# Performance work log

Hardware: AMD Instinct MI355X
Metric: run time of the kernel (lower is better)

## Reference

```python
import jax, jax.numpy as jnp
import numpy as np

N, D, H, B = 16384, 256, 4, 64
K_EDGE, TOP_K, NUM_HOPS = 3, 5, 2
EDGE_THRESH = 0.3
EPS = 1e-8


def setup_inputs() -> dict:
    key = jax.random.key(0)
    ks = jax.random.split(key, 32)
    g = lambda i, shape, sc=1.0: jax.random.normal(ks[i], shape, jnp.float32) * sc
    # sparse-ish symmetric adjacency (avg ~33 nonzeros/row, like a pruned memory graph)
    adj = jax.random.uniform(ks[0], (N, N), jnp.float32)
    adj = adj * (jax.random.uniform(ks[1], (N, N), jnp.float32) < 0.002)
    adj = jnp.maximum(adj, adj.T)
    return dict(
        nodes=g(2, (N, D)),
        node_values=g(3, (N,)),
        adjacency=adj,
        related_pos=g(4, (B, D)),
        query=g(5, (B, D)),
        w_in=g(6, (3 * D, D), D ** -0.5),
        b_in=jnp.zeros((3 * D,), jnp.float32),
        w_out=g(7, (D, D), D ** -0.5),
        b_out=jnp.zeros((D,), jnp.float32),
        rel_w1=g(8, (2 * D, D), (2 * D) ** -0.5),
        rel_b1=jnp.zeros((D,), jnp.float32),
        rel_w2=g(9, (D, D // 2), D ** -0.5),
        rel_b2=jnp.zeros((D // 2,), jnp.float32),
        rel_w3=g(10, (D // 2, 1), (D // 2) ** -0.5),
        rel_b3=jnp.zeros((1,), jnp.float32),
        gru_w_ih=g(11, (3 * D, D), D ** -0.5),
        gru_w_hh=g(12, (3 * D, D), D ** -0.5),
        gru_b_ih=jnp.zeros((3 * D,), jnp.float32),
        gru_b_hh=jnp.zeros((3 * D,), jnp.float32),
        node_timestamps=jax.random.randint(ks[13], (N,), 0, N),
        write_idx=jax.random.randint(ks[14], (B,), 0, N),
        total_writes=N,
    )


def _l2n(x):
    return x / (jnp.linalg.norm(x, axis=-1, keepdims=True) + EPS)


def reference(nodes, node_values, adjacency, related_pos, query,
              w_in, b_in, w_out, b_out,
              rel_w1, rel_b1, rel_w2, rel_b2, rel_w3, rel_b3,
              gru_w_ih, gru_w_hh, gru_b_ih, gru_b_hh,
              node_timestamps, write_idx, total_writes):
    b, d = query.shape
    n = nodes.shape[0]
    dh = d // H
    nodes_n = _l2n(nodes)

    # ---- write path: cosine-sim top-k edge scoring + relation-encoder MLP ----
    sims_w = _l2n(related_pos) @ nodes_n.T                      # [B,N]
    _, nbr = jax.lax.top_k(sims_w, K_EDGE)                      # [B,K]
    src = nodes[write_idx]                                      # [B,D]
    dst = nodes[nbr]                                            # [B,K,D]
    comb = jnp.concatenate(
        [jnp.broadcast_to(src[:, None, :], dst.shape), dst], -1)  # [B,K,2D]
    h = jax.nn.relu(comb @ rel_w1 + rel_b1)
    h = jax.nn.relu(h @ rel_w2 + rel_b2)
    strength = jax.nn.sigmoid(h @ rel_w3 + rel_b3)[..., 0]     # [B,K]
    same = nbr == write_idx[:, None]
    old = adjacency[write_idx[:, None], nbr]
    val = jnp.where(same, old, strength)                        # skip self-edges
    adj2 = adjacency.at[write_idx[:, None], nbr].set(val)
    adj2 = adj2.at[nbr, write_idx[:, None]].set(val)            # symmetric write

    # ---- retrieval: weighted cosine similarity + top-k seeds ----
    sims = _l2n(query) @ nodes_n.T                              # [B,N]
    recency = jnp.exp(-0.01 * (total_writes - node_timestamps).astype(jnp.float32))
    weighted = sims * jax.nn.sigmoid(node_values) * recency
    _, seed = jax.lax.top_k(weighted, TOP_K)                    # [B,TOP_K]
    visited = jnp.zeros((b, n), bool).at[jnp.arange(b)[:, None], seed].set(True)

    # ---- multi-hop graph expansion over thresholded adjacency ----
    adj_bool = (adj2 > EDGE_THRESH).astype(jnp.float32)
    for _ in range(NUM_HOPS):
        visited = visited | ((visited.astype(jnp.float32) @ adj_bool) > 0)

    # ---- masked multi-head attention: query attends to visited nodes ----
    q = (query @ w_in[:d].T + b_in[:d]).reshape(b, H, dh)
    k = (nodes @ w_in[d:2 * d].T + b_in[d:2 * d]).reshape(n, H, dh)
    v = (nodes @ w_in[2 * d:].T + b_in[2 * d:]).reshape(n, H, dh)
    scores = jnp.einsum('bhd,nhd->bhn', q, k) / np.float32(np.sqrt(dh))
    scores = jnp.where(visited[:, None, :], scores, jnp.float32(-1e9))
    attn = jax.nn.softmax(scores, axis=-1)
    ctx = jnp.einsum('bhn,nhd->bhd', attn, v).reshape(b, d)
    attended = ctx @ w_out.T + b_out                            # [B,D]

    # ---- GRUCell memory evolution: x=query, h=attended ----
    gi = query @ gru_w_ih.T + gru_b_ih
    gh = attended @ gru_w_hh.T + gru_b_hh
    i_r, i_z, i_n = jnp.split(gi, 3, -1)
    h_r, h_z, h_n = jnp.split(gh, 3, -1)
    r = jax.nn.sigmoid(i_r + h_r)
    z = jax.nn.sigmoid(i_z + h_z)
    nn_ = jnp.tanh(i_n + r * h_n)
    evolved = (1.0 - z) * nn_ + z * attended                    # [B,D]
    return evolved
```

## Files before the change

kernel.cpp:

```cpp
#include <hip/hip_runtime.h>
#include <math.h>
#include <stdint.h>

#define NN 16384
#define DD 256
#define ETH 0.3f
#define EDGE_CAP (4*1024*1024)

typedef unsigned long long u64;
typedef uint32_t u32;
typedef float f32x4 __attribute__((ext_vector_type(4)));

__global__ __launch_bounds__(256) void node_stats_k(const float* __restrict__ nodes,
    const float* __restrict__ nv, const int* __restrict__ ts, const int* __restrict__ tw,
    float* __restrict__ inv_norm, float* __restrict__ sal){
  int row = blockIdx.x*4 + (threadIdx.x>>6);
  int lane = threadIdx.x & 63;
  const float4* r4 = (const float4*)(nodes + (size_t)row*DD);
  float4 v = r4[lane];
  float s = v.x*v.x+v.y*v.y+v.z*v.z+v.w*v.w;
  #pragma unroll
  for (int o=32;o>0;o>>=1) s += __shfl_down(s,o);
  if (lane==0){
    inv_norm[row] = 1.0f/(sqrtf(s)+1e-8f);
    float x = nv[row];
    float sig = 1.0f/(1.0f+expf(-x));
    float rec = expf(-0.01f*(float)(tw[0]-ts[row]));
    sal[row] = sig*rec;
  }
}

__global__ __launch_bounds__(64) void norm_qr_k(const float* __restrict__ query,
    const float* __restrict__ related, float* __restrict__ qr){
  int blk = blockIdx.x; int lane = threadIdx.x;
  const float* src = (blk<64)? (related + (size_t)blk*DD) : (query + (size_t)(blk-64)*DD);
  float4 v = ((const float4*)src)[lane];
  float s = v.x*v.x+v.y*v.y+v.z*v.z+v.w*v.w;
  #pragma unroll
  for (int o=32;o>0;o>>=1) s += __shfl_down(s,o);
  s = __shfl(s,0);
  float inv = 1.0f/(sqrtf(s)+1e-8f);
  ((float4*)(qr + (size_t)blk*DD))[lane] = make_float4(v.x*inv,v.y*inv,v.z*inv,v.w*inv);
}

#define ACC8(r) do{ \
    accA[r].x += qs*nv0.x; accA[r].y += qs*nv0.y; accA[r].z += qs*nv0.z; accA[r].w += qs*nv0.w; \
    accB[r].x += qs*nv1.x; accB[r].y += qs*nv1.y; accB[r].z += qs*nv1.z; accB[r].w += qs*nv1.w; }while(0)

template<int RM>
__global__ __launch_bounds__(256) void gemm_smallM_k(const float* __restrict__ Qm,
    const float* __restrict__ nodes, float* __restrict__ out0, float* __restrict__ out1,
    const float* __restrict__ inv_norm, const float* __restrict__ sal, int mode){
  constexpr int M = RM*32;
  constexpr int KC = 32;
  __shared__ float qk[KC*M];
  __shared__ float ndk[KC*64];
  int t = threadIdx.x;
  int qg = t>>3, ng = t&7;
  int n0 = blockIdx.x*64;
  float4 accA[RM], accB[RM];
  #pragma unroll
  for (int r=0;r<RM;r++){ accA[r]=make_float4(0,0,0,0); accB[r]=make_float4(0,0,0,0); }
  for (int kb=0; kb<DD; kb+=KC){
    if (t < M){
      const float4* src = (const float4*)(Qm + (size_t)t*DD + kb);
      #pragma unroll
      for (int i=0;i<KC/4;i++){
        float4 w = src[i];
        qk[(i*4+0)*M+t]=w.x; qk[(i*4+1)*M+t]=w.y;
        qk[(i*4+2)*M+t]=w.z; qk[(i*4+3)*M+t]=w.w;
      }
    }
    {
      int nn = t&63, kq = t>>6;
      const float4* src = (const float4*)(nodes + (size_t)(n0+nn)*DD + kb + kq*8);
      float4 a = src[0], b = src[1];
      ndk[(kq*8+0)*64+nn]=a.x; ndk[(kq*8+1)*64+nn]=a.y; ndk[(kq*8+2)*64+nn]=a.z; ndk[(kq*8+3)*64+nn]=a.w;
      ndk[(kq*8+4)*64+nn]=b.x; ndk[(kq*8+5)*64+nn]=b.y; ndk[(kq*8+6)*64+nn]=b.z; ndk[(kq*8+7)*64+nn]=b.w;
    }
    __syncthreads();
    for (int k=0;k<KC;k++){
      float4 nv0 = *(const float4*)&ndk[k*64 + ng*8];
      float4 nv1 = *(const float4*)&ndk[k*64 + ng*8 + 4];
      float4 q0  = *(const float4*)&qk[k*M + qg*RM];
      float qs;
      qs=q0.x; ACC8(0); qs=q0.y; ACC8(1); qs=q0.z; ACC8(2); qs=q0.w; ACC8(3);
      if constexpr (RM==8){
        float4 q1 = *(const float4*)&qk[k*M + qg*RM + 4];
        qs=q1.x; ACC8(4); qs=q1.y; ACC8(5); qs=q1.z; ACC8(6); qs=q1.w; ACC8(7);
      }
    }
    __syncthreads();
  }
  int nbase = n0 + ng*8;
  float4 in0, in1, sa0, sa1;
  if (mode==0){
    in0 = *(const float4*)&inv_norm[nbase]; in1 = *(const float4*)&inv_norm[nbase+4];
    sa0 = *(const float4*)&sal[nbase];      sa1 = *(const float4*)&sal[nbase+4];
  }
  #pragma unroll
  for (int r=0;r<RM;r++){
    int row = qg*RM + r;
    float4 a = accA[r], b = accB[r];
    if (mode==0){
      float4 s0 = make_float4(a.x*in0.x, a.y*in0.y, a.z*in0.z, a.w*in0.w);
      float4 s1 = make_float4(b.x*in1.x, b.y*in1.y, b.z*in1.z, b.w*in1.w);
      if (row < 64){
        *(float4*)&out0[(size_t)row*NN + nbase]     = s0;
        *(float4*)&out0[(size_t)row*NN + nbase + 4] = s1;
      } else {
        float4 w0 = make_float4(s0.x*sa0.x, s0.y*sa0.y, s0.z*sa0.z, s0.w*sa0.w);
        float4 w1 = make_float4(s1.x*sa1.x, s1.y*sa1.y, s1.z*sa1.z, s1.w*sa1.w);
        *(float4*)&out1[(size_t)(row-64)*NN + nbase]     = w0;
        *(float4*)&out1[(size_t)(row-64)*NN + nbase + 4] = w1;
      }
    } else {
      float4 s0 = make_float4(a.x*0.125f, a.y*0.125f, a.z*0.125f, a.w*0.125f);
      float4 s1 = make_float4(b.x*0.125f, b.y*0.125f, b.z*0.125f, b.w*0.125f);
      *(float4*)&out0[(size_t)row*NN + nbase]     = s0;
      *(float4*)&out0[(size_t)row*NN + nbase + 4] = s1;
    }
  }
}

__global__ __launch_bounds__(1024) void topk_k(const float* __restrict__ src, int K,
    int* __restrict__ outIdx, u64* __restrict__ vis){
  int b = blockIdx.x, t = threadIdx.x;
  const float* row = src + (size_t)b*NN;
  __shared__ float sv[1024]; __shared__ int si[1024]; __shared__ int chosen[5];
  for (int kk=0;kk<K;kk++){
    float best = -3.0e38f; int bi = NN;
    for (int n=t;n<NN;n+=1024){
      bool skip=false;
      for (int c=0;c<kk;c++) if (chosen[c]==n) skip=true;
      if (skip) continue;
      float v = row[n];
      if (v > best){ best=v; bi=n; }
    }
    sv[t]=best; si[t]=bi;
    __syncthreads();
    for (int s=512;s>0;s>>=1){
      if (t<s){
        float v2=sv[t+s]; int i2=si[t+s];
        if (v2>sv[t] || (v2==sv[t] && i2<si[t])){ sv[t]=v2; si[t]=i2; }
      }
      __syncthreads();
    }
    if (t==0){
      chosen[kk]=si[0]; outIdx[b*K+kk]=si[0];
      if (vis) atomicOr(&vis[si[0]], 1ull<<b);
    }
    __syncthreads();
  }
}

__global__ __launch_bounds__(256) void rel_patch_k(const float* __restrict__ nodes,
    const int* __restrict__ write_idx, const int* __restrict__ nbr,
    const float* __restrict__ w1, const float* __restrict__ b1,
    const float* __restrict__ w2, const float* __restrict__ b2,
    const float* __restrict__ w3, const float* __restrict__ b3,
    u32* __restrict__ modkeys, u32* __restrict__ addkeys, int* __restrict__ ctrl,
    u32* __restrict__ rowmod){
  int b = blockIdx.x, t = threadIdx.x;
  __shared__ float comb[512], h1[256], red[128];
  int w = write_idx[b];
  for (int k=0;k<3;k++){
    int nb = nbr[b*3+k];
    comb[t]     = nodes[(size_t)w*DD + t];
    comb[256+t] = nodes[(size_t)nb*DD + t];
    __syncthreads();
    float a1 = b1[t];
    for (int i=0;i<512;i++) a1 += comb[i]*w1[(size_t)i*256 + t];
    h1[t] = a1>0.f ? a1 : 0.f;
    __syncthreads();
    if (t<128){
      float a2 = b2[t];
      for (int i=0;i<256;i++) a2 += h1[i]*w2[(size_t)i*128 + t];
      float h2 = a2>0.f ? a2 : 0.f;
      red[t] = h2*w3[t];
    }
    __syncthreads();
    for (int s=64;s>0;s>>=1){ if (t<s) red[t]+=red[t+s]; __syncthreads(); }
    if (t==0 && nb != w){
      float strength = 1.0f/(1.0f+expf(-(red[0]+b3[0])));
      u32 k1 = ((u32)w<<14)|(u32)nb, k2 = ((u32)nb<<14)|(u32)w;
      int m = atomicAdd(&ctrl[1],2);
      modkeys[m]=k1; modkeys[m+1]=k2;
      if (strength > ETH){ int a=atomicAdd(&ctrl[2],2); addkeys[a]=k1; addkeys[a+1]=k2; }
      atomicOr(&rowmod[(u32)w>>5], 1u<<((u32)w&31));
      atomicOr(&rowmod[(u32)nb>>5], 1u<<((u32)nb&31));
    }
    __syncthreads();
  }
}

#define LCAP 4096
#define GITER 8
__global__ __launch_bounds__(256) void scan_adj_k(const float* __restrict__ adj,
    const u32* __restrict__ rowmod, const u32* __restrict__ modkeys,
    const int* __restrict__ ctrl, u32* __restrict__ edges, int* __restrict__ ecnt){
  __shared__ u32 lbuf[LCAP];
  __shared__ int lcnt, gbase;
  int t = threadIdx.x;
  if (t==0) lcnt = 0;
  __syncthreads();
  int nm = ctrl[1];
  size_t tid = (size_t)blockIdx.x*256 + t;
  size_t stride = (size_t)gridDim.x*256;
  const f32x4* a4 = (const f32x4*)adj;
  const size_t total4 = (size_t)NN*NN/4;
  int iters = (int)(total4 / stride);
  for (int g=0; g<iters; g+=GITER){
    f32x4 x0,x1,x2,x3,x4,x5,x6,x7;
    asm volatile("global_load_dwordx4 %0, %1, off" : "=v"(x0) : "v"(a4 + tid + (size_t)(g+0)*stride));
    asm volatile("global_load_dwordx4 %0, %1, off" : "=v"(x1) : "v"(a4 + tid + (size_t)(g+1)*stride));
    asm volatile("global_load_dwordx4 %0, %1, off" : "=v"(x2) : "v"(a4 + tid + (size_t)(g+2)*stride));
    asm volatile("global_load_dwordx4 %0, %1, off" : "=v"(x3) : "v"(a4 + tid + (size_t)(g+3)*stride));
    asm volatile("global_load_dwordx4 %0, %1, off" : "=v"(x4) : "v"(a4 + tid + (size_t)(g+4)*stride));
    asm volatile("global_load_dwordx4 %0, %1, off" : "=v"(x5) : "v"(a4 + tid + (size_t)(g+5)*stride));
    asm volatile("global_load_dwordx4 %0, %1, off" : "=v"(x6) : "v"(a4 + tid + (size_t)(g+6)*stride));
    asm volatile("global_load_dwordx4 %0, %1, off" : "=v"(x7) : "v"(a4 + tid + (size_t)(g+7)*stride));
    asm volatile("s_waitcnt vmcnt(0)" ::: "memory");
    __builtin_amdgcn_sched_barrier(0);
    #define PROC(XX, GI) do{ \
      _Pragma("unroll") \
      for (int e=0;e<4;e++){ \
        if (XX[e] > ETH){ \
          size_t li = (tid + (size_t)(g+GI)*stride)*4 + e; \
          u32 i = (u32)(li >> 14), j = (u32)(li & 16383); \
          u32 key = (i<<14)|j; \
          bool keep = true; \
          if ((rowmod[i>>5]>>(i&31))&1u){ \
            for (int c=0;c<nm;c++) if (modkeys[c]==key){ keep=false; break; } \
          } \
          if (keep){ \
            int p = atomicAdd(&lcnt, 1); \
            if (p < LCAP) lbuf[p] = key; \
            else { int d = atomicAdd(ecnt,1); if (d < EDGE_CAP) edges[d] = key; } \
          } \
        } \
      } }while(0)
    PROC(x0,0); PROC(x1,1); PROC(x2,2); PROC(x3,3);
    PROC(x4,4); PROC(x5,5); PROC(x6,6); PROC(x7,7);
    #undef PROC
  }
  __syncthreads();
  int cnt = lcnt; if (cnt > LCAP) cnt = LCAP;
  if (cnt > 0){
    if (t==0) gbase = atomicAdd(ecnt, cnt);
    __syncthreads();
    int b0 = gbase;
    for (int i=t; i<cnt; i+=256){
      int d = b0 + i;
      if (d < EDGE_CAP) edges[d] = lbuf[i];
    }
  }
}

__global__ void patch_add_k(const u32* __restrict__ addkeys, const int* __restrict__ ctrl,
    u32* __restrict__ edges, int* __restrict__ ecnt){
  if (blockIdx.x==0 && threadIdx.x==0){
    int na = ctrl[2];
    int base = atomicAdd(ecnt, na);
    for (int i=0;i<na;i++) if (base+i < EDGE_CAP) edges[base+i] = addkeys[i];
  }
}

__global__ __launch_bounds__(256) void propagate_k(const u32* __restrict__ edges,
    const int* __restrict__ ecnt, const u64* __restrict__ vin, u64* __restrict__ vout){
  int n = *ecnt; if (n > EDGE_CAP) n = EDGE_CAP;
  int tid = blockIdx.x*256 + threadIdx.x;
  int stride = gridDim.x*256;
  for (int idx=tid; idx<n; idx+=stride){
    u32 key = edges[idx];
    u32 i = key>>14, j = key & 16383u;
    u64 wv = vin[i];
    if (wv) atomicOr(&vout[j], wv);
  }
}

__global__ __launch_bounds__(256) void qproj_k(const float* __restrict__ query,
    const float* __restrict__ w_in, const float* __restrict__ b_in, float* __restrict__ qproj){
  int b = blockIdx.x, o = threadIdx.x;
  float s = b_in[o];
  const float* wr = w_in + (size_t)o*256;
  const float* q = query + (size_t)b*256;
  for (int c=0;c<256;c++) s += q[c]*wr[c];
  qproj[b*256+o]=s;
}

__global__ __launch_bounds__(256) void qw_k(const float* __restrict__ qproj,
    const float* __restrict__ w_in, float* __restrict__ qW){
  int r = blockIdx.x;
  int c = threadIdx.x;
  int b = r>>2, hh = r&3;
  float s=0.f;
  for (int dh=0; dh<64; dh++)
    s += qproj[b*256 + hh*64 + dh] * w_in[(size_t)(256 + hh*64 + dh)*256 + c];
  qW[(size_t)r*256+c]=s;
}

__global__ __launch_bounds__(256) void softmax_k(float* __restrict__ scores, const u64* __restrict__ vis){
  int r = blockIdx.x; int bb = r >> 2; int t = threadIdx.x;
  float* row = scores + (size_t)r*NN;
  __shared__ float red[256];
  float mx = -3.0e38f;
  for (int n=t; n<NN; n+=256)
    if ((vis[n]>>bb)&1ull) mx = fmaxf(mx, row[n]);
  red[t]=mx; __syncthreads();
  for (int s=128;s>0;s>>=1){ if (t<s) red[t]=fmaxf(red[t],red[t+s]); __syncthreads(); }
  mx = red[0]; __syncthreads();
  float sum=0.f;
  for (int n=t;n<NN;n+=256)
    if ((vis[n]>>bb)&1ull) sum += expf(row[n]-mx);
  red[t]=sum; __syncthreads();
  for (int s=128;s>0;s>>=1){ if (t<s) red[t]+=red[t+s]; __syncthreads(); }
  float inv = 1.0f/red[0];
  for (int n=t;n<NN;n+=256){
    float v = 0.f;
    if ((vis[n]>>bb)&1ull) v = expf(row[n]-mx)*inv;
    row[n]=v;
  }
}

__global__ __launch_bounds__(256) void agg_k(const float* __restrict__ attn,
    const float* __restrict__ nodes, float* __restrict__ partial){
  int c = blockIdx.x;
  int h = blockIdx.y;
  int t = threadIdx.x;
  int bb = t >> 2, qq = t & 3;
  __shared__ float att[64*129];
  float4 acc[16];
  #pragma unroll
  for (int i=0;i<16;i++) acc[i] = make_float4(0.f,0.f,0.f,0.f);
  for (int sub=0; sub<2; sub++){
    int n0 = c*256 + sub*128;
    __syncthreads();
    for (int idx=t; idx<64*128; idx+=256){
      int rb = idx>>7, nn = idx&127;
      att[rb*129+nn] = attn[((size_t)(rb*4+h))*NN + n0 + nn];
    }
    __syncthreads();
    for (int nn=0; nn<128; nn++){
      float a = att[bb*129+nn];
      const float4* nr = (const float4*)(nodes + ((size_t)(n0+nn))*DD + qq*64);
      #pragma unroll
      for (int i=0;i<16;i++){
        float4 x = nr[i];
        acc[i].x += a*x.x; acc[i].y += a*x.y; acc[i].z += a*x.z; acc[i].w += a*x.w;
      }
    }
  }
  float* dst = partial + (((size_t)(c*4+h)*64 + bb)*256) + qq*64;
  #pragma unroll
  for (int i=0;i<16;i++) ((float4*)dst)[i] = acc[i];
}

__global__ __launch_bounds__(256) void reduce_partial_k(const float* __restrict__ partial,
    float* __restrict__ ctxraw){
  int idx = blockIdx.x*256 + threadIdx.x;
  int d = idx & 255; int bh = idx >> 8;
  int hh = bh & 3, b = bh >> 2;
  float s=0.f;
  for (int c=0;c<64;c++) s += partial[(((size_t)c*4+hh)*64 + b)*256 + d];
  ctxraw[idx] = s;
}

__global__ __launch_bounds__(256) void ctx_k(const float* __restrict__ ctxraw,
    const float* __restrict__ w_in, const float* __restrict__ b_in, float* __restrict__ ctx){
  int b = blockIdx.x, o = threadIdx.x;
  int hh = o >> 6;
  const float* cr = ctxraw + (size_t)(b*4+hh)*256;
  const float* wr = w_in + (size_t)(512+o)*256;
  float s = b_in[512+o];
  for (int d=0; d<256; d++) s += cr[d]*wr[d];
  ctx[b*256+o] = s;
}

__global__ __launch_bounds__(256) void attended_k(const float* __restrict__ ctx,
    const float* __restrict__ w_out, const float* __restrict__ b_out, float* __restrict__ att){
  int b = blockIdx.x, o = threadIdx.x;
  const float* cr = ctx + (size_t)b*256;
  const float* wr = w_out + (size_t)o*256;
  float s = b_out[o];
  for (int c=0;c<256;c++) s += cr[c]*wr[c];
  att[b*256+o] = s;
}

__global__ __launch_bounds__(256) void gru_k(const float* __restrict__ query,
    const float* __restrict__ att, const float* __restrict__ w_ih, const float* __restrict__ w_hh,
    const float* __restrict__ b_ih, const float* __restrict__ b_hh, float* __restrict__ out){
  int b = blockIdx.x, o = threadIdx.x;
  const float* q = query + (size_t)b*256;
  const float* a = att + (size_t)b*256;
  float ir=b_ih[o], iz=b_ih[256+o], inn=b_ih[512+o];
  float hr=b_hh[o], hz=b_hh[256+o], hn=b_hh[512+o];
  for (int c=0;c<256;c++){
    float qc=q[c], ac=a[c];
    ir += qc*w_ih[(size_t)o*256+c];
    iz += qc*w_ih[(size_t)(256+o)*256+c];
    inn+= qc*w_ih[(size_t)(512+o)*256+c];
    hr += ac*w_hh[(size_t)o*256+c];
    hz += ac*w_hh[(size_t)(256+o)*256+c];
    hn += ac*w_hh[(size_t)(512+o)*256+c];
  }
  float r = 1.f/(1.f+expf(-(ir+hr)));
  float z = 1.f/(1.f+expf(-(iz+hz)));
  float nval = tanhf(inn + r*hn);
  out[b*256+o] = (1.f-z)*nval + z*a[o];
}

extern "C" void kernel_launch(void* const* d_in, const int* in_sizes, int n_in,
                              void* d_out, int out_size, void* d_ws, size_t ws_size,
                              hipStream_t stream){
  (void)in_sizes; (void)n_in; (void)out_size; (void)ws_size;
  const float* nodes     = (const float*)d_in[0];
  const float* node_vals = (const float*)d_in[1];
  const float* adjacency = (const float*)d_in[2];
  const float* related   = (const float*)d_in[3];
  const float* query     = (const float*)d_in[4];
  const float* w_in      = (const float*)d_in[5];
  const float* b_in      = (const float*)d_in[6];
  const float* w_out     = (const float*)d_in[7];
  const float* b_out     = (const float*)d_in[8];
  const float* rel_w1    = (const float*)d_in[9];
  const float* rel_b1    = (const float*)d_in[10];
  const float* rel_w2    = (const float*)d_in[11];
  const float* rel_b2    = (const float*)d_in[12];
  const float* rel_w3    = (const float*)d_in[13];
  const float* rel_b3    = (const float*)d_in[14];
  const float* gw_ih     = (const float*)d_in[15];
  const float* gw_hh     = (const float*)d_in[16];
  const float* gb_ih     = (const float*)d_in[17];
  const float* gb_hh     = (const float*)d_in[18];
  const int*   ts        = (const int*)d_in[19];
  const int*   write_idx = (const int*)d_in[20];
  const int*   tw        = (const int*)d_in[21];
  float* out = (float*)d_out;

  char* ws = (char*)d_ws;
  size_t off = 0;
  auto alloc = [&](size_t bytes)->char*{
    char* p = ws + off; off += (bytes + 255) & ~(size_t)255; return p;
  };
  float* inv_norm = (float*)alloc(NN*4);
  float* sal      = (float*)alloc(NN*4);
  float* qr       = (float*)alloc(128*DD*4);
  float* simw     = (float*)alloc((size_t)64*NN*4);
  float* wsims    = (float*)alloc((size_t)64*NN*4);
  int*   nbr      = (int*)  alloc(64*3*4);
  int*   seed     = (int*)  alloc(64*5*4);
  float* qproj    = (float*)alloc(64*256*4);
  float* qW       = (float*)alloc(256*256*4);
  float* scores   = (float*)alloc((size_t)256*NN*4);
  float* ctxraw   = (float*)alloc(64*4*256*4);
  float* ctx      = (float*)alloc(64*256*4);
  float* attended = (float*)alloc(64*256*4);
  u64*   V0       = (u64*)  alloc(NN*8);
  u64*   V1       = (u64*)  alloc(NN*8);
  u32*   edges    = (u32*)  alloc((size_t)EDGE_CAP*4);
  float* partial  = (float*)edges;
  int*   ctrl     = (int*)  alloc(256);
  u32*   modkeys  = (u32*)  alloc(512*4);
  u32*   addkeys  = (u32*)  alloc(512*4);
  u32*   rowmod   = (u32*)  alloc(NN/8);

  hipMemsetAsync(ctrl, 0, 256, stream);
  hipMemsetAsync(rowmod, 0, NN/8, stream);
  hipMemsetAsync(V0, 0, NN*8, stream);

  node_stats_k<<<NN/4, 256, 0, stream>>>(nodes, node_vals, ts, tw, inv_norm, sal);
  norm_qr_k<<<128, 64, 0, stream>>>(query, related, qr);
  gemm_smallM_k<4><<<NN/64, 256, 0, stream>>>(qr, nodes, simw, wsims, inv_norm, sal, 0);
  topk_k<<<64, 1024, 0, stream>>>(simw, 3, nbr, (u64*)nullptr);
  topk_k<<<64, 1024, 0, stream>>>(wsims, 5, seed, V0);
  rel_patch_k<<<64, 256, 0, stream>>>(nodes, write_idx, nbr, rel_w1, rel_b1, rel_w2, rel_b2,
                                      rel_w3, rel_b3, modkeys, addkeys, ctrl, rowmod);
  scan_adj_k<<<2048, 256, 0, stream>>>(adjacency, rowmod, modkeys, ctrl, edges, &ctrl[0]);
  patch_add_k<<<1, 64, 0, stream>>>(addkeys, ctrl, edges, &ctrl[0]);
  hipMemcpyAsync(V1, V0, NN*8, hipMemcpyDeviceToDevice, stream);
  propagate_k<<<1024, 256, 0, stream>>>(edges, &ctrl[0], V0, V1);
  hipMemcpyAsync(V0, V1, NN*8, hipMemcpyDeviceToDevice, stream);
  propagate_k<<<1024, 256, 0, stream>>>(edges, &ctrl[0], V1, V0);
  qproj_k<<<64, 256, 0, stream>>>(query, w_in, b_in, qproj);
  qw_k<<<256, 256, 0, stream>>>(qproj, w_in, qW);
  gemm_smallM_k<8><<<NN/64, 256, 0, stream>>>(qW, nodes, scores, (float*)nullptr,
                                              (const float*)nullptr, (const float*)nullptr, 1);
  softmax_k<<<256, 256, 0, stream>>>(scores, V0);
  agg_k<<<dim3(64,4), 256, 0, stream>>>(scores, nodes, partial);
  reduce_partial_k<<<256, 256, 0, stream>>>(partial, ctxraw);
  ctx_k<<<64, 256, 0, stream>>>(ctxraw, w_in, b_in, ctx);
  attended_k<<<64, 256, 0, stream>>>(ctx, w_out, b_out, attended);
  gru_k<<<64, 256, 0, stream>>>(query, attended, gw_ih, gw_hh, gb_ih, gb_hh, out);
}
```

Before: 1.468 ms.

## Double-buffer adjacency scan loads and fold softmax normalization into aggregation

The adjacency scan now keeps two banks of eight 16-byte loads in flight and waits on only the older bank, so the next group's memory traffic overlaps the current group's threshold checks. The softmax pass is replaced by an online max/sum row-statistics kernel that writes no probabilities. The aggregation kernel applies the visited mask and exp-normalization while staging scores into shared memory, which removes one read pass and one write pass over the scores matrix. The cost is more live registers in the scan kernel, which may lower occupancy, and the use of the faster __expf approximation.

```diff
diff --git a/kernel.cpp b/kernel.cpp
--- a/kernel.cpp
+++ b/kernel.cpp
@@ -196,6 +196,39 @@
 
 #define LCAP 4096
 #define GITER 8
+#define ISSUE(P, GB) do{ \
+  asm volatile("global_load_dwordx4 %0, %1, off" : "=v"(P##0) : "v"(a4 + tid + (size_t)((GB)+0)*stride)); \
+  asm volatile("global_load_dwordx4 %0, %1, off" : "=v"(P##1) : "v"(a4 + tid + (size_t)((GB)+1)*stride)); \
+  asm volatile("global_load_dwordx4 %0, %1, off" : "=v"(P##2) : "v"(a4 + tid + (size_t)((GB)+2)*stride)); \
+  asm volatile("global_load_dwordx4 %0, %1, off" : "=v"(P##3) : "v"(a4 + tid + (size_t)((GB)+3)*stride)); \
+  asm volatile("global_load_dwordx4 %0, %1, off" : "=v"(P##4) : "v"(a4 + tid + (size_t)((GB)+4)*stride)); \
+  asm volatile("global_load_dwordx4 %0, %1, off" : "=v"(P##5) : "v"(a4 + tid + (size_t)((GB)+5)*stride)); \
+  asm volatile("global_load_dwordx4 %0, %1, off" : "=v"(P##6) : "v"(a4 + tid + (size_t)((GB)+6)*stride)); \
+  asm volatile("global_load_dwordx4 %0, %1, off" : "=v"(P##7) : "v"(a4 + tid + (size_t)((GB)+7)*stride)); \
+}while(0)
+#define PROC1(XX, GI) do{ \
+  _Pragma("unroll") \
+  for (int e=0;e<4;e++){ \
+    if (XX[e] > ETH){ \
+      size_t li = (tid + (size_t)(GI)*stride)*4 + e; \
+      u32 i = (u32)(li >> 14), j = (u32)(li & 16383); \
+      u32 key = (i<<14)|j; \
+      bool keep = true; \
+      if ((rowmod[i>>5]>>(i&31))&1u){ \
+        for (int c=0;c<nm;c++) if (modkeys[c]==key){ keep=false; break; } \
+      } \
+      if (keep){ \
+        int p = atomicAdd(&lcnt, 1); \
+        if (p < LCAP) lbuf[p] = key; \
+        else { int d = atomicAdd(ecnt,1); if (d < EDGE_CAP) edges[d] = key; } \
+      } \
+    } \
+  } }while(0)
+#define PROC8(P, GB) do{ \
+  PROC1(P##0,(GB)+0); PROC1(P##1,(GB)+1); PROC1(P##2,(GB)+2); PROC1(P##3,(GB)+3); \
+  PROC1(P##4,(GB)+4); PROC1(P##5,(GB)+5); PROC1(P##6,(GB)+6); PROC1(P##7,(GB)+7); \
+}while(0)
+
 __global__ __launch_bounds__(256) void scan_adj_k(const float* __restrict__ adj,
     const u32* __restrict__ rowmod, const u32* __restrict__ modkeys,
     const int* __restrict__ ctrl, u32* __restrict__ edges, int* __restrict__ ecnt){
@@ -209,40 +242,24 @@
   size_t stride = (size_t)gridDim.x*256;
   const f32x4* a4 = (const f32x4*)adj;
   const size_t total4 = (size_t)NN*NN/4;
-  int iters = (int)(total4 / stride);
-  for (int g=0; g<iters; g+=GITER){
-    f32x4 x0,x1,x2,x3,x4,x5,x6,x7;
-    asm volatile("global_load_dwordx4 %0, %1, off" : "=v"(x0) : "v"(a4 + tid + (size_t)(g+0)*stride));
-    asm volatile("global_load_dwordx4 %0, %1, off" : "=v"(x1) : "v"(a4 + tid + (size_t)(g+1)*stride));
-    asm volatile("global_load_dwordx4 %0, %1, off" : "=v"(x2) : "v"(a4 + tid + (size_t)(g+2)*stride));
-    asm volatile("global_load_dwordx4 %0, %1, off" : "=v"(x3) : "v"(a4 + tid + (size_t)(g+3)*stride));
-    asm volatile("global_load_dwordx4 %0, %1, off" : "=v"(x4) : "v"(a4 + tid + (size_t)(g+4)*stride));
-    asm volatile("global_load_dwordx4 %0, %1, off" : "=v"(x5) : "v"(a4 + tid + (size_t)(g+5)*stride));
-    asm volatile("global_load_dwordx4 %0, %1, off" : "=v"(x6) : "v"(a4 + tid + (size_t)(g+6)*stride));
-    asm volatile("global_load_dwordx4 %0, %1, off" : "=v"(x7) : "v"(a4 + tid + (size_t)(g+7)*stride));
-    asm volatile("s_waitcnt vmcnt(0)" ::: "memory");
+  const int iters = (int)(total4 / stride);
+  f32x4 xa0,xa1,xa2,xa3,xa4,xa5,xa6,xa7;
+  f32x4 xb0,xb1,xb2,xb3,xb4,xb5,xb6,xb7;
+  ISSUE(xa, 0);
+  #pragma unroll 1
+  for (int g=0; g<iters; g+=2*GITER){
+    ISSUE(xb, g+GITER);
+    asm volatile("s_waitcnt vmcnt(8)" ::: "memory");
     __builtin_amdgcn_sched_barrier(0);
-    #define PROC(XX, GI) do{ \
-      _Pragma("unroll") \
-      for (int e=0;e<4;e++){ \
-        if (XX[e] > ETH){ \
-          size_t li = (tid + (size_t)(g+GI)*stride)*4 + e; \
-          u32 i = (u32)(li >> 14), j = (u32)(li & 16383); \
-          u32 key = (i<<14)|j; \
-          bool keep = true; \
-          if ((rowmod[i>>5]>>(i&31))&1u){ \
-            for (int c=0;c<nm;c++) if (modkeys[c]==key){ keep=false; break; } \
-          } \
-          if (keep){ \
-            int p = atomicAdd(&lcnt, 1); \
-            if (p < LCAP) lbuf[p] = key; \
-            else { int d = atomicAdd(ecnt,1); if (d < EDGE_CAP) edges[d] = key; } \
-          } \
-        } \
-      } }while(0)
-    PROC(x0,0); PROC(x1,1); PROC(x2,2); PROC(x3,3);
-    PROC(x4,4); PROC(x5,5); PROC(x6,6); PROC(x7,7);
-    #undef PROC
+    PROC8(xa, g);
+    if (g + 2*GITER < iters){
+      ISSUE(xa, g+2*GITER);
+      asm volatile("s_waitcnt vmcnt(8)" ::: "memory");
+    } else {
+      asm volatile("s_waitcnt vmcnt(0)" ::: "memory");
+    }
+    __builtin_amdgcn_sched_barrier(0);
+    PROC8(xb, g+GITER);
   }
   __syncthreads();
   int cnt = lcnt; if (cnt > LCAP) cnt = LCAP;
@@ -300,36 +317,42 @@
   qW[(size_t)r*256+c]=s;
 }
 
-__global__ __launch_bounds__(256) void softmax_k(float* __restrict__ scores, const u64* __restrict__ vis){
+__global__ __launch_bounds__(256) void rowstat_k(const float* __restrict__ scores,
+    const u64* __restrict__ vis, float* __restrict__ m_out, float* __restrict__ is_out){
   int r = blockIdx.x; int bb = r >> 2; int t = threadIdx.x;
-  float* row = scores + (size_t)r*NN;
-  __shared__ float red[256];
-  float mx = -3.0e38f;
-  for (int n=t; n<NN; n+=256)
-    if ((vis[n]>>bb)&1ull) mx = fmaxf(mx, row[n]);
-  red[t]=mx; __syncthreads();
-  for (int s=128;s>0;s>>=1){ if (t<s) red[t]=fmaxf(red[t],red[t+s]); __syncthreads(); }
-  mx = red[0]; __syncthreads();
-  float sum=0.f;
-  for (int n=t;n<NN;n+=256)
-    if ((vis[n]>>bb)&1ull) sum += expf(row[n]-mx);
-  red[t]=sum; __syncthreads();
-  for (int s=128;s>0;s>>=1){ if (t<s) red[t]+=red[t+s]; __syncthreads(); }
-  float inv = 1.0f/red[0];
-  for (int n=t;n<NN;n+=256){
-    float v = 0.f;
-    if ((vis[n]>>bb)&1ull) v = expf(row[n]-mx)*inv;
-    row[n]=v;
-  }
+  const float* row = scores + (size_t)r*NN;
+  float m = -3.0e38f, s = 0.f;
+  for (int n=t; n<NN; n+=256){
+    if ((vis[n]>>bb)&1ull){
+      float v = row[n];
+      if (v > m){ s = s*__expf(m - v) + 1.0f; m = v; }
+      else s += __expf(v - m);
+    }
+  }
+  __shared__ float sm[256], ss[256];
+  sm[t]=m; ss[t]=s; __syncthreads();
+  for (int st=128; st>0; st>>=1){
+    if (t<st){
+      float m2=sm[t+st], s2=ss[t+st];
+      float mm = fmaxf(sm[t], m2);
+      ss[t] = ss[t]*__expf(sm[t]-mm) + s2*__expf(m2-mm);
+      sm[t] = mm;
+    }
+    __syncthreads();
+  }
+  if (t==0){ m_out[r] = sm[0]; is_out[r] = 1.0f/ss[0]; }
 }
 
 __global__ __launch_bounds__(256) void agg_k(const float* __restrict__ attn,
-    const float* __restrict__ nodes, float* __restrict__ partial){
+    const float* __restrict__ m_in, const float* __restrict__ is_in,
+    const u64* __restrict__ vis, const float* __restrict__ nodes, float* __restrict__ partial){
   int c = blockIdx.x;
   int h = blockIdx.y;
   int t = threadIdx.x;
   int bb = t >> 2, qq = t & 3;
   __shared__ float att[64*129];
+  __shared__ float smx[64], sis[64];
+  if (t < 64){ smx[t] = m_in[t*4+h]; sis[t] = is_in[t*4+h]; }
   float4 acc[16];
   #pragma unroll
   for (int i=0;i<16;i++) acc[i] = make_float4(0.f,0.f,0.f,0.f);
@@ -338,7 +361,10 @@
     __syncthreads();
     for (int idx=t; idx<64*128; idx+=256){
       int rb = idx>>7, nn = idx&127;
-      att[rb*129+nn] = attn[((size_t)(rb*4+h))*NN + n0 + nn];
+      int node = n0 + nn;
+      float raw = attn[((size_t)(rb*4+h))*NN + node];
+      float p = ((vis[node]>>rb)&1ull) ? __expf(raw - smx[rb])*sis[rb] : 0.f;
+      att[rb*129+nn] = p;
     }
     __syncthreads();
     for (int nn=0; nn<128; nn++){
@@ -453,6 +479,8 @@
   float* qproj    = (float*)alloc(64*256*4);
   float* qW       = (float*)alloc(256*256*4);
   float* scores   = (float*)alloc((size_t)256*NN*4);
+  float* m_row    = (float*)alloc(256*4);
+  float* is_row   = (float*)alloc(256*4);
   float* ctxraw   = (float*)alloc(64*4*256*4);
   float* ctx      = (float*)alloc(64*256*4);
   float* attended = (float*)alloc(64*256*4);
@@ -486,8 +514,8 @@
   qw_k<<<256, 256, 0, stream>>>(qproj, w_in, qW);
   gemm_smallM_k<8><<<NN/64, 256, 0, stream>>>(qW, nodes, scores, (float*)nullptr,
                                               (const float*)nullptr, (const float*)nullptr, 1);
-  softmax_k<<<256, 256, 0, stream>>>(scores, V0);
-  agg_k<<<dim3(64,4), 256, 0, stream>>>(scores, nodes, partial);
+  rowstat_k<<<256, 256, 0, stream>>>(scores, V0, m_row, is_row);
+  agg_k<<<dim3(64,4), 256, 0, stream>>>(scores, m_row, is_row, V0, nodes, partial);
   reduce_partial_k<<<256, 256, 0, stream>>>(partial, ctxraw);
   ctx_k<<<64, 256, 0, stream>>>(ctxraw, w_in, b_in, ctx);
   attended_k<<<64, 256, 0, stream>>>(ctx, w_out, b_out, attended);
```

Result: no change. 1.472 ms (+0.3%).
